# Kernel optimization log

Hardware: AMD Instinct MI355X
Metric: run time of the kernel (lower is better)

## Reference

```python
import jax, jax.numpy as jnp
import numpy as np

NUM_STAGES = 2
DE_NEIGHBORS = 3

def _square_distance(a, b):
    # a: [B,N,3], b: [B,S,3] -> [B,N,S] squared euclidean distances
    return (jnp.sum(a * a, axis=-1)[:, :, None]
            + jnp.sum(b * b, axis=-1)[:, None, :]
            - 2.0 * jnp.einsum('bnc,bsc->bns', a, b))

def _propagate(xyz1, xyz2, points1, points2, k):
    # xyz1:[B,N,3] fine, xyz2:[B,S,3] coarse, points1:[B,D1,N], points2:[B,D2,S]
    p2 = jnp.transpose(points2, (0, 2, 1))  # [B,S,D2]
    B, N, _ = xyz1.shape
    S = xyz2.shape[1]
    if S == 1:
        interp = jnp.broadcast_to(p2, (B, N, p2.shape[-1]))
    else:
        d = _square_distance(xyz1, xyz2)              # [B,N,S]
        neg_top, idx = jax.lax.top_k(-d, k)           # k smallest distances
        dists = -neg_top                              # [B,N,k]
        recip = 1.0 / (dists + 1e-8)
        weight = recip / jnp.sum(recip, axis=2, keepdims=True)  # [B,N,k]
        # gather neighbor features: [B,N,k,D2]
        gathered = jnp.take_along_axis(p2[:, None, :, :], idx[..., None], axis=2)
        interp = jnp.sum(gathered * weight[..., None], axis=2)  # [B,N,D2]
    if points1 is not None:
        p1 = jnp.transpose(points1, (0, 2, 1))        # [B,N,D1]
        new = jnp.concatenate([p1, interp], axis=-1)
    else:
        new = interp
    return jnp.transpose(new, (0, 2, 1))              # [B,D1+D2,N]

def setup_inputs() -> dict:
    key = jax.random.key(0)
    ks = jax.random.split(key, 6)
    return {
        'xyz0': jax.random.normal(ks[0], (4, 8192, 3), dtype=jnp.float32),
        'xyz1': jax.random.normal(ks[1], (4, 2048, 3), dtype=jnp.float32),
        'xyz2': jax.random.normal(ks[2], (4, 512, 3), dtype=jnp.float32),
        'x0': jax.random.normal(ks[3], (4, 128, 8192), dtype=jnp.float32),
        'x1': jax.random.normal(ks[4], (4, 256, 2048), dtype=jnp.float32),
        'x2': jax.random.normal(ks[5], (4, 512, 512), dtype=jnp.float32),
    }

def reference(xyz0, xyz1, xyz2, x0, x1, x2):
    # original forward reverses the lists; emulate with pre-reversed lists
    xyz_list = [xyz2, xyz1, xyz0]   # coarse -> fine
    x_list = [x2, x1, x0]
    x = x_list[0]
    for i in range(NUM_STAGES):
        x = _propagate(xyz_list[i + 1], xyz_list[i], x_list[i + 1], x, DE_NEIGHBORS)
    return x  # [4, 896, 8192]
```

## Files before the change

kernel.cpp:

```cpp
#include <hip/hip_runtime.h>

#define BIG 3.0e38f

__device__ __forceinline__ void insert3(float d, int s,
                                        float& d0, float& d1, float& d2,
                                        int& i0, int& i1, int& i2) {
    const bool b0 = d < d0;
    const bool b1 = d < d1;
    const bool b2 = d < d2;
    d2 = b1 ? d1 : (b2 ? d : d2);
    i2 = b1 ? i1 : (b2 ? s : i2);
    d1 = b0 ? d0 : (b1 ? d : d1);
    i1 = b0 ? i0 : (b1 ? s : i1);
    d0 = b0 ? d : d0;
    i0 = b0 ? s : i0;
}

template <int S>
__device__ void knn_tile(const float* __restrict__ xyzF, const float* __restrict__ xyzC,
                         int N, int b, int nb,
                         int* __restrict__ idx, float* __restrict__ w,
                         void* smem) {
    constexpr int SPC = S / 8;
    float4* sc  = (float4*)smem;
    float*  smd = (float*)((char*)smem + S * 16);
    int*    smi = (int*)((char*)smem + S * 16 + 3072);
    const int tid = threadIdx.x;

    for (int i = tid; i < S; i += 256) {
        const float x = xyzC[(b * S + i) * 3 + 0];
        const float y = xyzC[(b * S + i) * 3 + 1];
        const float z = xyzC[(b * S + i) * 3 + 2];
        sc[i] = make_float4(x, y, z, x * x + y * y + z * z);
    }
    __syncthreads();

    const int q  = tid & 31;
    const int sp = tid >> 5;
    const int n  = nb + q;
    const float ax = xyzF[(b * N + n) * 3 + 0];
    const float ay = xyzF[(b * N + n) * 3 + 1];
    const float az = xyzF[(b * N + n) * 3 + 2];
    const float an = ax * ax + ay * ay + az * az;

    float d0 = BIG, d1 = BIG, d2 = BIG;
    int i0 = 0, i1 = 0, i2 = 0;
    const int s0 = sp * SPC;
#pragma unroll 8
    for (int s = s0; s < s0 + SPC; ++s) {
        const float4 p = sc[s];
        const float t = ax * p.x + ay * p.y + az * p.z;
        const float d = an + p.w - 2.0f * t;
        insert3(d, s, d0, d1, d2, i0, i1, i2);
    }

    smd[tid * 3 + 0] = d0; smi[tid * 3 + 0] = i0;
    smd[tid * 3 + 1] = d1; smi[tid * 3 + 1] = i1;
    smd[tid * 3 + 2] = d2; smi[tid * 3 + 2] = i2;
    __syncthreads();

    if (tid < 32) {
        float e0 = BIG, e1 = BIG, e2 = BIG;
        int j0 = 0, j1 = 0, j2 = 0;
#pragma unroll
        for (int ch = 0; ch < 8; ++ch) {
#pragma unroll
            for (int k = 0; k < 3; ++k) {
                insert3(smd[(ch * 32 + tid) * 3 + k], smi[(ch * 32 + tid) * 3 + k],
                        e0, e1, e2, j0, j1, j2);
            }
        }
        const float r0 = 1.0f / (e0 + 1e-8f);
        const float r1 = 1.0f / (e1 + 1e-8f);
        const float r2 = 1.0f / (e2 + 1e-8f);
        const float rs = r0 + r1 + r2;
        const int nn = nb + tid;
        idx[(b * 3 + 0) * N + nn] = j0;
        idx[(b * 3 + 1) * N + nn] = j1;
        idx[(b * 3 + 2) * N + nn] = j2;
        w[(b * 3 + 0) * N + nn] = r0 / rs;
        w[(b * 3 + 1) * N + nn] = r1 / rs;
        w[(b * 3 + 2) * N + nn] = r2 / rs;
    }
}

__device__ void transpose_tile(const float* __restrict__ in, float* __restrict__ out,
                               int C, int N, int OS, int co,
                               int b, int nb, int cb, void* smem) {
    float (*s)[65] = (float (*)[65])smem;
    const int lo = threadIdx.x & 63;
    const int r  = threadIdx.x >> 6;
#pragma unroll
    for (int i = 0; i < 16; ++i) {
        const int cl = r + 4 * i;
        s[cl][lo] = in[((size_t)b * C + cb + cl) * N + nb + lo];
    }
    __syncthreads();
#pragma unroll
    for (int i = 0; i < 16; ++i) {
        const int pl = r + 4 * i;
        out[((size_t)b * N + nb + pl) * OS + co + cb + lo] = s[lo][pl];
    }
}

__device__ void interp1_tile(const float* __restrict__ x2P,
                             const int* __restrict__ idx, const float* __restrict__ w,
                             float* __restrict__ featP,
                             int b, int nb, int cb, void* smem) {
    int*   sj = (int*)smem;
    float* sw = (float*)((char*)smem + 768);
    const int tid = threadIdx.x;

    if (tid < 64) {
#pragma unroll
        for (int k = 0; k < 3; ++k) {
            sj[k * 64 + tid] = idx[(b * 3 + k) * 2048 + nb + tid];
            sw[k * 64 + tid] = w[(b * 3 + k) * 2048 + nb + tid];
        }
    }
    __syncthreads();

    const int c = tid & 63, r = tid >> 6;
#pragma unroll
    for (int i = 0; i < 16; ++i) {
        const int p = r + 4 * i;
        const float v = sw[0 * 64 + p] * x2P[((size_t)b * 512 + sj[0 * 64 + p]) * 512 + cb + c]
                      + sw[1 * 64 + p] * x2P[((size_t)b * 512 + sj[1 * 64 + p]) * 512 + cb + c]
                      + sw[2 * 64 + p] * x2P[((size_t)b * 512 + sj[2 * 64 + p]) * 512 + cb + c];
        featP[((size_t)b * 2048 + nb + p) * 768 + 256 + cb + c] = v;
    }
}

__global__ __launch_bounds__(256) void k1_stage(const float* __restrict__ xyz1,
                                                const float* __restrict__ xyz2,
                                                const float* __restrict__ x2,
                                                float* __restrict__ x2P,
                                                int* __restrict__ idx1,
                                                float* __restrict__ w1) {
    __shared__ float4 smem4[1040];
    const int id = blockIdx.x;
    if (id < 256) {
        const int b  = id >> 6;
        const int nb = (id & 63) * 32;
        knn_tile<512>(xyz1, xyz2, 2048, b, nb, idx1, w1, smem4);
    } else {
        const int r  = id - 256;
        const int b  = r >> 6;
        const int nb = (r & 7) * 64;
        const int cb = ((r >> 3) & 7) * 64;
        transpose_tile(x2, x2P, 512, 512, 512, 0, b, nb, cb, smem4);
    }
}

__global__ __launch_bounds__(256) void k2_stage(const float* __restrict__ xyz0,
                                                const float* __restrict__ xyz1,
                                                const float* __restrict__ x0,
                                                const float* __restrict__ x1,
                                                const float* __restrict__ x2P,
                                                const int* __restrict__ idx1,
                                                const float* __restrict__ w1,
                                                float* __restrict__ featP,
                                                int* __restrict__ idx2,
                                                float* __restrict__ w2,
                                                float* __restrict__ out) {
    __shared__ float4 smem4[2432];
    const int id = blockIdx.x;
    if (id < 1024) {
        const int b  = id >> 8;
        const int nb = (id & 255) * 32;
        knn_tile<2048>(xyz0, xyz1, 8192, b, nb, idx2, w2, smem4);
    } else if (id < 2048) {
        const int r  = id - 1024;
        const int b  = r >> 8;
        const int nb = (r & 31) * 64;
        const int cb = ((r >> 5) & 7) * 64;
        interp1_tile(x2P, idx1, w1, featP, b, nb, cb, smem4);
    } else if (id < 2560) {
        const int r  = id - 2048;
        const int b  = r >> 7;
        const int nb = (r & 31) * 64;
        const int cb = ((r >> 5) & 3) * 64;
        transpose_tile(x1, featP, 256, 2048, 768, 0, b, nb, cb, smem4);
    } else {
        const int r  = id - 2560;
        const int b  = r >> 6;
        const int lb = r & 63;
        const float4* src = (const float4*)x0;
        float4* dst = (float4*)out;
#pragma unroll
        for (int t = 0; t < 16; ++t) {
            const int i = lb * 4096 + t * 256 + threadIdx.x;
            dst[(size_t)b * (896 * 2048) + i] = src[(size_t)b * (128 * 2048) + i];
        }
    }
}

__global__ __launch_bounds__(256) void final_interp(const float* __restrict__ featP,
                                                    const int* __restrict__ idx,
                                                    const float* __restrict__ w,
                                                    float* __restrict__ out) {
    __shared__ float tile[64][65];
    __shared__ int   sj[3][64];
    __shared__ float sw[3][64];
    const int b = blockIdx.y;
    const int id = blockIdx.x;
    const int ntile = (id & 7) * 16 + ((id >> 3) & 15);
    const int ctile = id >> 7;
    const int nb = ntile * 64;
    const int cb = ctile * 64;
    const int tid = threadIdx.x;

    if (tid < 64) {
#pragma unroll
        for (int k = 0; k < 3; ++k) {
            sj[k][tid] = idx[(b * 3 + k) * 8192 + nb + tid];
            sw[k][tid] = w[(b * 3 + k) * 8192 + nb + tid];
        }
    }
    __syncthreads();

    {
        const int c = tid & 63, r = tid >> 6;
#pragma unroll
        for (int i = 0; i < 16; ++i) {
            const int p = r + 4 * i;
            const float v = sw[0][p] * featP[((size_t)b * 2048 + sj[0][p]) * 768 + cb + c]
                          + sw[1][p] * featP[((size_t)b * 2048 + sj[1][p]) * 768 + cb + c]
                          + sw[2][p] * featP[((size_t)b * 2048 + sj[2][p]) * 768 + cb + c];
            tile[p][c] = v;
        }
    }
    __syncthreads();
    {
        const int p = tid & 63, r = tid >> 6;
#pragma unroll
        for (int i = 0; i < 16; ++i) {
            const int cl = r + 4 * i;
            out[((size_t)b * 896 + 128 + cb + cl) * 8192 + nb + p] = tile[p][cl];
        }
    }
}

extern "C" void kernel_launch(void* const* d_in, const int* in_sizes, int n_in,
                              void* d_out, int out_size, void* d_ws, size_t ws_size,
                              hipStream_t stream) {
    const float* xyz0 = (const float*)d_in[0];
    const float* xyz1 = (const float*)d_in[1];
    const float* xyz2 = (const float*)d_in[2];
    const float* x0   = (const float*)d_in[3];
    const float* x1   = (const float*)d_in[4];
    const float* x2   = (const float*)d_in[5];
    float* out = (float*)d_out;

    char* ws = (char*)d_ws;
    float* featP = (float*)(ws + 0);
    int*   idx1  = (int*)(ws + 25165824);
    float* w1    = (float*)(ws + 25264128);
    int*   idx2  = (int*)(ws + 25362432);
    float* w2    = (float*)(ws + 25755648);
    float* x2P   = (float*)(ws + 26148864);

    k1_stage<<<dim3(512), 256, 0, stream>>>(xyz1, xyz2, x2, x2P, idx1, w1);
    k2_stage<<<dim3(2816), 256, 0, stream>>>(xyz0, xyz1, x0, x1, x2P, idx1, w1,
                                             featP, idx2, w2, out);
    final_interp<<<dim3(1536, 4), 256, 0, stream>>>(featP, idx2, w2, out);
}
```

Measured before the change: 218.1 us.

## Compose two-level interpolation weights and merge kernels, dropping intermediate featP

The intermediate interpolated feature tensor featP (2048 points x 768 channels) is no longer materialised. The final kernel now composes the two 3-NN stages into 9 neighbours with product weights and gathers directly from the transposed coarse features x2P. Both kNN stages, the transposes and the x0 copy are merged into one launch, so there are two kernels instead of three. This removes a large intermediate write and read and one launch, but the upper channel blocks now do 9 gathers per output instead of 3 and load their indices through a dependent lookup chain.

```diff
diff --git a/kernel.cpp b/kernel.cpp
--- a/kernel.cpp
+++ b/kernel.cpp
@@ -85,7 +85,7 @@
 }
 
 __device__ void transpose_tile(const float* __restrict__ in, float* __restrict__ out,
-                               int C, int N, int OS, int co,
+                               int C, int N, int OS,
                                int b, int nb, int cb, void* smem) {
     float (*s)[65] = (float (*)[65])smem;
     const int lo = threadIdx.x & 63;
@@ -99,67 +99,20 @@
 #pragma unroll
     for (int i = 0; i < 16; ++i) {
         const int pl = r + 4 * i;
-        out[((size_t)b * N + nb + pl) * OS + co + cb + lo] = s[lo][pl];
-    }
-}
-
-__device__ void interp1_tile(const float* __restrict__ x2P,
-                             const int* __restrict__ idx, const float* __restrict__ w,
-                             float* __restrict__ featP,
-                             int b, int nb, int cb, void* smem) {
-    int*   sj = (int*)smem;
-    float* sw = (float*)((char*)smem + 768);
-    const int tid = threadIdx.x;
-
-    if (tid < 64) {
-#pragma unroll
-        for (int k = 0; k < 3; ++k) {
-            sj[k * 64 + tid] = idx[(b * 3 + k) * 2048 + nb + tid];
-            sw[k * 64 + tid] = w[(b * 3 + k) * 2048 + nb + tid];
-        }
-    }
-    __syncthreads();
-
-    const int c = tid & 63, r = tid >> 6;
-#pragma unroll
-    for (int i = 0; i < 16; ++i) {
-        const int p = r + 4 * i;
-        const float v = sw[0 * 64 + p] * x2P[((size_t)b * 512 + sj[0 * 64 + p]) * 512 + cb + c]
-                      + sw[1 * 64 + p] * x2P[((size_t)b * 512 + sj[1 * 64 + p]) * 512 + cb + c]
-                      + sw[2 * 64 + p] * x2P[((size_t)b * 512 + sj[2 * 64 + p]) * 512 + cb + c];
-        featP[((size_t)b * 2048 + nb + p) * 768 + 256 + cb + c] = v;
-    }
-}
-
-__global__ __launch_bounds__(256) void k1_stage(const float* __restrict__ xyz1,
+        out[((size_t)b * N + nb + pl) * OS + cb + lo] = s[lo][pl];
+    }
+}
+
+__global__ __launch_bounds__(256) void k1_stage(const float* __restrict__ xyz0,
+                                                const float* __restrict__ xyz1,
                                                 const float* __restrict__ xyz2,
+                                                const float* __restrict__ x0,
+                                                const float* __restrict__ x1,
                                                 const float* __restrict__ x2,
+                                                float* __restrict__ x1P,
                                                 float* __restrict__ x2P,
                                                 int* __restrict__ idx1,
-                                                float* __restrict__ w1) {
-    __shared__ float4 smem4[1040];
-    const int id = blockIdx.x;
-    if (id < 256) {
-        const int b  = id >> 6;
-        const int nb = (id & 63) * 32;
-        knn_tile<512>(xyz1, xyz2, 2048, b, nb, idx1, w1, smem4);
-    } else {
-        const int r  = id - 256;
-        const int b  = r >> 6;
-        const int nb = (r & 7) * 64;
-        const int cb = ((r >> 3) & 7) * 64;
-        transpose_tile(x2, x2P, 512, 512, 512, 0, b, nb, cb, smem4);
-    }
-}
-
-__global__ __launch_bounds__(256) void k2_stage(const float* __restrict__ xyz0,
-                                                const float* __restrict__ xyz1,
-                                                const float* __restrict__ x0,
-                                                const float* __restrict__ x1,
-                                                const float* __restrict__ x2P,
-                                                const int* __restrict__ idx1,
-                                                const float* __restrict__ w1,
-                                                float* __restrict__ featP,
+                                                float* __restrict__ w1,
                                                 int* __restrict__ idx2,
                                                 float* __restrict__ w2,
                                                 float* __restrict__ out) {
@@ -169,20 +122,25 @@
         const int b  = id >> 8;
         const int nb = (id & 255) * 32;
         knn_tile<2048>(xyz0, xyz1, 8192, b, nb, idx2, w2, smem4);
+    } else if (id < 1280) {
+        const int r  = id - 1024;
+        const int b  = r >> 6;
+        const int nb = (r & 63) * 32;
+        knn_tile<512>(xyz1, xyz2, 2048, b, nb, idx1, w1, smem4);
+    } else if (id < 1536) {
+        const int r  = id - 1280;
+        const int b  = r >> 6;
+        const int nb = (r & 7) * 64;
+        const int cb = ((r >> 3) & 7) * 64;
+        transpose_tile(x2, x2P, 512, 512, 512, b, nb, cb, smem4);
     } else if (id < 2048) {
-        const int r  = id - 1024;
-        const int b  = r >> 8;
-        const int nb = (r & 31) * 64;
-        const int cb = ((r >> 5) & 7) * 64;
-        interp1_tile(x2P, idx1, w1, featP, b, nb, cb, smem4);
-    } else if (id < 2560) {
-        const int r  = id - 2048;
+        const int r  = id - 1536;
         const int b  = r >> 7;
         const int nb = (r & 31) * 64;
         const int cb = ((r >> 5) & 3) * 64;
-        transpose_tile(x1, featP, 256, 2048, 768, 0, b, nb, cb, smem4);
+        transpose_tile(x1, x1P, 256, 2048, 256, b, nb, cb, smem4);
     } else {
-        const int r  = id - 2560;
+        const int r  = id - 2048;
         const int b  = r >> 6;
         const int lb = r & 63;
         const float4* src = (const float4*)x0;
@@ -195,48 +153,92 @@
     }
 }
 
-__global__ __launch_bounds__(256) void final_interp(const float* __restrict__ featP,
-                                                    const int* __restrict__ idx,
-                                                    const float* __restrict__ w,
-                                                    float* __restrict__ out) {
+__global__ __launch_bounds__(256) void final_fused(const float* __restrict__ x1P,
+                                                   const float* __restrict__ x2P,
+                                                   const int* __restrict__ idx1,
+                                                   const float* __restrict__ w1,
+                                                   const int* __restrict__ idx2,
+                                                   const float* __restrict__ w2,
+                                                   float* __restrict__ out) {
     __shared__ float tile[64][65];
-    __shared__ int   sj[3][64];
-    __shared__ float sw[3][64];
+    __shared__ int   sj[9][64];
+    __shared__ float sw[9][64];
     const int b = blockIdx.y;
     const int id = blockIdx.x;
     const int ntile = (id & 7) * 16 + ((id >> 3) & 15);
     const int ctile = id >> 7;
     const int nb = ntile * 64;
-    const int cb = ctile * 64;
     const int tid = threadIdx.x;
 
-    if (tid < 64) {
-#pragma unroll
-        for (int k = 0; k < 3; ++k) {
-            sj[k][tid] = idx[(b * 3 + k) * 8192 + nb + tid];
-            sw[k][tid] = w[(b * 3 + k) * 8192 + nb + tid];
-        }
-    }
-    __syncthreads();
-
-    {
-        const int c = tid & 63, r = tid >> 6;
-#pragma unroll
-        for (int i = 0; i < 16; ++i) {
-            const int p = r + 4 * i;
-            const float v = sw[0][p] * featP[((size_t)b * 2048 + sj[0][p]) * 768 + cb + c]
-                          + sw[1][p] * featP[((size_t)b * 2048 + sj[1][p]) * 768 + cb + c]
-                          + sw[2][p] * featP[((size_t)b * 2048 + sj[2][p]) * 768 + cb + c];
-            tile[p][c] = v;
-        }
-    }
-    __syncthreads();
-    {
-        const int p = tid & 63, r = tid >> 6;
-#pragma unroll
-        for (int i = 0; i < 16; ++i) {
-            const int cl = r + 4 * i;
-            out[((size_t)b * 896 + 128 + cb + cl) * 8192 + nb + p] = tile[p][cl];
+    if (ctile < 4) {
+        if (tid < 64) {
+#pragma unroll
+            for (int k = 0; k < 3; ++k) {
+                sj[k][tid] = idx2[(b * 3 + k) * 8192 + nb + tid];
+                sw[k][tid] = w2[(b * 3 + k) * 8192 + nb + tid];
+            }
+        }
+        __syncthreads();
+        const int cb = ctile * 64;
+        {
+            const int c = tid & 63, r = tid >> 6;
+            const float* xb = x1P + (size_t)b * 2048 * 256 + cb + c;
+#pragma unroll
+            for (int i = 0; i < 16; ++i) {
+                const int p = r + 4 * i;
+                const float v = sw[0][p] * xb[(size_t)sj[0][p] * 256]
+                              + sw[1][p] * xb[(size_t)sj[1][p] * 256]
+                              + sw[2][p] * xb[(size_t)sj[2][p] * 256];
+                tile[p][c] = v;
+            }
+        }
+        __syncthreads();
+        {
+            const int p = tid & 63, r = tid >> 6;
+#pragma unroll
+            for (int i = 0; i < 16; ++i) {
+                const int cl = r + 4 * i;
+                out[((size_t)b * 896 + 128 + cb + cl) * 8192 + nb + p] = tile[p][cl];
+            }
+        }
+    } else {
+        if (tid < 64) {
+            const int n = nb + tid;
+#pragma unroll
+            for (int k = 0; k < 3; ++k) {
+                const int   j  = idx2[(b * 3 + k) * 8192 + n];
+                const float wk = w2[(b * 3 + k) * 8192 + n];
+#pragma unroll
+                for (int m = 0; m < 3; ++m) {
+                    sj[k * 3 + m][tid] = idx1[(b * 3 + m) * 2048 + j];
+                    sw[k * 3 + m][tid] = wk * w1[(b * 3 + m) * 2048 + j];
+                }
+            }
+        }
+        __syncthreads();
+        const int cb = (ctile - 4) * 64;
+        {
+            const int c = tid & 63, r = tid >> 6;
+            const float* xb = x2P + (size_t)b * 512 * 512 + cb + c;
+#pragma unroll
+            for (int i = 0; i < 16; ++i) {
+                const int p = r + 4 * i;
+                float v = 0.0f;
+#pragma unroll
+                for (int j = 0; j < 9; ++j) {
+                    v += sw[j][p] * xb[(size_t)sj[j][p] * 512];
+                }
+                tile[p][c] = v;
+            }
+        }
+        __syncthreads();
+        {
+            const int p = tid & 63, r = tid >> 6;
+#pragma unroll
+            for (int i = 0; i < 16; ++i) {
+                const int cl = r + 4 * i;
+                out[((size_t)b * 896 + 384 + cb + cl) * 8192 + nb + p] = tile[p][cl];
+            }
         }
     }
 }
@@ -253,15 +255,14 @@
     float* out = (float*)d_out;
 
     char* ws = (char*)d_ws;
-    float* featP = (float*)(ws + 0);
-    int*   idx1  = (int*)(ws + 25165824);
-    float* w1    = (float*)(ws + 25264128);
-    int*   idx2  = (int*)(ws + 25362432);
-    float* w2    = (float*)(ws + 25755648);
-    float* x2P   = (float*)(ws + 26148864);
-
-    k1_stage<<<dim3(512), 256, 0, stream>>>(xyz1, xyz2, x2, x2P, idx1, w1);
-    k2_stage<<<dim3(2816), 256, 0, stream>>>(xyz0, xyz1, x0, x1, x2P, idx1, w1,
-                                             featP, idx2, w2, out);
-    final_interp<<<dim3(1536, 4), 256, 0, stream>>>(featP, idx2, w2, out);
-}
+    float* x1P  = (float*)(ws + 0);
+    float* x2P  = (float*)(ws + 8388608);
+    int*   idx1 = (int*)(ws + 12582912);
+    float* w1   = (float*)(ws + 12681216);
+    int*   idx2 = (int*)(ws + 12779520);
+    float* w2   = (float*)(ws + 13172736);
+
+    k1_stage<<<dim3(2304), 256, 0, stream>>>(xyz0, xyz1, xyz2, x0, x1, x2,
+                                             x1P, x2P, idx1, w1, idx2, w2, out);
+    final_fused<<<dim3(1536, 4), 256, 0, stream>>>(x1P, x2P, idx1, w1, idx2, w2, out);
+}
```

Measured after the change: 213.9 us. Within noise of the previous version (-1.9%).
